# Optimization experiments

Hardware: AMD Instinct MI355X
Metric: run time of the kernel (lower is better)

Reference implementation:

```python
import jax, jax.numpy as jnp
import numpy as np

# Straight-through sign binarization (Binarize in BNN code mutates .data, so
# autograd sees identity -> custom_vjp with identity backward).
@jax.custom_vjp
def binarize(x):
    return jnp.sign(x)

def _bin_fwd(x):
    return jnp.sign(x), None

def _bin_bwd(_, g):
    return (g,)

binarize.defvjp(_bin_fwd, _bin_bwd)

EPS = 1e-5  # torch BatchNorm1d default eps

def batchnorm(x, g, b):
    # training-mode BN: batch statistics, biased variance
    if x.ndim == 3:  # (N, C, L): stats over N and L
        m = x.mean(axis=(0, 2), keepdims=True)
        v = x.var(axis=(0, 2), keepdims=True)
        return (x - m) / jnp.sqrt(v + EPS) * g[None, :, None] + b[None, :, None]
    m = x.mean(axis=0)
    v = x.var(axis=0)
    return (x - m) / jnp.sqrt(v + EPS) * g + b

def hardtanh(x):
    return jnp.clip(x, -1.0, 1.0)

def maxpool3(x):
    # MaxPool1d(kernel=3, stride=3): trim then reshape-max
    N, C, L = x.shape
    Lp = L // 3
    return x[:, :, :Lp * 3].reshape(N, C, Lp, 3).max(axis=-1)

def bconv(x, w, b, binarize_input=True):
    # BinarizeConv1d: kernel 41, dilation 2, VALID padding; weights sign-binarized,
    # inputs binarized except when in_channels == 3 (first layer rule in BNN code).
    xb = binarize(x) if binarize_input else x
    wb = binarize(w)
    y = jax.lax.conv_general_dilated(
        xb, wb, window_strides=(1,), padding='VALID',
        rhs_dilation=(2,), dimension_numbers=('NCH', 'OIH', 'NCH'))
    return y + b[None, :, None]

def blinear(x, w, b):
    # BinarizeLinear: in_features 832/1024 != 784 -> binarize input and weight
    return binarize(x) @ binarize(w).T + b

def _forward(x, bn0_g, bn0_b, conv1_w, conv1_b, bn1_g, bn1_b,
             conv2_w, conv2_b, bn2_g, bn2_b, conv3_w, conv3_b,
             bn3_g, bn3_b, conv4_w, conv4_b, bn4_g, bn4_b,
             conv5_w, conv5_b, fc1_w, fc1_b, bn5_g, bn5_b,
             fc2_w, fc2_b, bn6_g, bn6_b):
    h = hardtanh(batchnorm(x, bn0_g, bn0_b))
    h = maxpool3(bconv(h, conv1_w, conv1_b, binarize_input=False))  # (N,64,5306)
    h = hardtanh(batchnorm(h, bn1_g, bn1_b))
    h = maxpool3(bconv(h, conv2_w, conv2_b))  # (N,64,1742)
    h = hardtanh(batchnorm(h, bn2_g, bn2_b))
    h = maxpool3(bconv(h, conv3_w, conv3_b))  # (N,64,554)
    h = hardtanh(batchnorm(h, bn3_g, bn3_b))
    h = maxpool3(bconv(h, conv4_w, conv4_b))  # (N,64,158)
    h = hardtanh(batchnorm(h, bn4_g, bn4_b))
    h = maxpool3(bconv(h, conv5_w, conv5_b))  # (N,32,26)
    h = h.reshape(-1, 16 * 52)                # (N, 832)
    h = hardtanh(batchnorm(blinear(h, fc1_w, fc1_b), bn5_g, bn5_b))
    h = batchnorm(blinear(h, fc2_w, fc2_b), bn6_g, bn6_b)
    return jax.nn.log_softmax(h, axis=1)

def setup_inputs() -> dict:
    key = jax.random.key(0)
    ks = jax.random.split(key, 32)
    def rn(k, shape, s=0.1):
        return jax.random.normal(k, shape, dtype=jnp.float32) * s
    def bn_params(kg, kb, c):
        return 1.0 + rn(kg, (c,)), rn(kb, (c,))
    N, L, K = 64, 16000, 41
    d = {"x": jax.random.normal(ks[0], (N, 3, L), dtype=jnp.float32)}
    d["bn0_g"], d["bn0_b"] = bn_params(ks[1], ks[2], 3)
    d["conv1_w"], d["conv1_b"] = rn(ks[3], (64, 3, K)), rn(ks[4], (64,), 0.01)
    d["bn1_g"], d["bn1_b"] = bn_params(ks[5], ks[6], 64)
    d["conv2_w"], d["conv2_b"] = rn(ks[7], (64, 64, K)), rn(ks[8], (64,), 0.01)
    d["bn2_g"], d["bn2_b"] = bn_params(ks[9], ks[10], 64)
    d["conv3_w"], d["conv3_b"] = rn(ks[11], (64, 64, K)), rn(ks[12], (64,), 0.01)
    d["bn3_g"], d["bn3_b"] = bn_params(ks[13], ks[14], 64)
    d["conv4_w"], d["conv4_b"] = rn(ks[15], (64, 64, K)), rn(ks[16], (64,), 0.01)
    d["bn4_g"], d["bn4_b"] = bn_params(ks[17], ks[18], 64)
    d["conv5_w"], d["conv5_b"] = rn(ks[19], (32, 64, K)), rn(ks[20], (32,), 0.01)
    d["fc1_w"], d["fc1_b"] = rn(ks[21], (1024, 832)), rn(ks[22], (1024,), 0.01)
    d["bn5_g"], d["bn5_b"] = bn_params(ks[23], ks[24], 1024)
    d["fc2_w"], d["fc2_b"] = rn(ks[25], (1000, 1024)), rn(ks[26], (1000,), 0.01)
    d["bn6_g"], d["bn6_b"] = bn_params(ks[27], ks[28], 1000)
    return d

def reference(x, bn0_g, bn0_b, conv1_w, conv1_b, bn1_g, bn1_b,
              conv2_w, conv2_b, bn2_g, bn2_b, conv3_w, conv3_b,
              bn3_g, bn3_b, conv4_w, conv4_b, bn4_g, bn4_b,
              conv5_w, conv5_b, fc1_w, fc1_b, bn5_g, bn5_b,
              fc2_w, fc2_b, bn6_g, bn6_b):
    return _forward(x, bn0_g, bn0_b, conv1_w, conv1_b, bn1_g, bn1_b,
                    conv2_w, conv2_b, bn2_g, bn2_b, conv3_w, conv3_b,
                    bn3_g, bn3_b, conv4_w, conv4_b, bn4_g, bn4_b,
                    conv5_w, conv5_b, fc1_w, fc1_b, bn5_g, bn5_b,
                    fc2_w, fc2_b, bn6_g, bn6_b)
```

## Files before the change

### kernel.cpp

```cpp
#include <hip/hip_runtime.h>
#include <hip/hip_bf16.h>
#include <stdint.h>

typedef __hip_bfloat16 bf16;
typedef unsigned long long u64;
typedef unsigned short u16;

typedef __attribute__((ext_vector_type(8))) short bf16x8;
typedef __attribute__((ext_vector_type(4))) float f32x4;
typedef __attribute__((ext_vector_type(4))) int i32x4;

#define FIXCAP (1u << 20)
#define YQS 5312

static __device__ __forceinline__ float ldin(const void* p, long i, int f32) {
    return f32 ? ((const float*)p)[i] : __bfloat162float(((const bf16*)p)[i]);
}

static __device__ __forceinline__ i32x4 expand16_01(unsigned m) {
    union { int4 s; i32x4 v; } u;
    u.s.x = (int)((((m         & 0xFu) * 0x00204081u) & 0x01010101u));
    u.s.y = (int)((((m >> 4)  & 0xFu) * 0x00204081u) & 0x01010101u);
    u.s.z = (int)((((m >> 8)  & 0xFu) * 0x00204081u) & 0x01010101u);
    u.s.w = (int)((((m >> 12) & 0xFu) * 0x00204081u) & 0x01010101u);
    return u.v;
}

__global__ void k_probe(const void* x, unsigned* ctl) {
    int tid = threadIdx.x;
    int good = 0;
    for (int i = tid; i < 1024; i += 256) {
        float v = __bfloat162float(((const bf16*)x)[2 * i]);
        float a = fabsf(v);
        if (v == 0.0f || (isfinite(v) && a >= 1e-4f && a <= 100.0f)) good++;
    }
    __shared__ int s[256];
    s[tid] = good; __syncthreads();
    for (int st = 128; st > 0; st >>= 1) {
        if (tid < st) s[tid] += s[tid + st];
        __syncthreads();
    }
    if (tid == 0) { ctl[0] = 0u; ctl[1] = (s[0] >= 700) ? 0u : 1u; }
}

__global__ void k_sentinel(void* outv, const unsigned* ctl, float val) {
    int i = blockIdx.x * 256 + threadIdx.x;
    if (i >= 64000) return;
    if (ctl[1]) ((float*)outv)[i] = val;
    else ((bf16*)outv)[i] = __float2bfloat16(val);
}

__device__ __forceinline__ void pack_convw_task(const void* w, uint2* wp, int Co, int f32,
                                                int bx, int tid) {
    int t = bx * 256 + tid;
    if (t >= Co * 41) return;
    int co = t / 41, k = t % 41;
    unsigned w0 = 0, w1 = 0;
    for (int c = 0; c < 32; c++)
        if (ldin(w, (co * 64 + c) * 41 + k, f32) > 0.f) w0 |= (1u << c);
    for (int c = 0; c < 32; c++)
        if (ldin(w, (co * 64 + 32 + c) * 41 + k, f32) > 0.f) w1 |= (1u << c);
    wp[t] = make_uint2(w0, w1);
}
__device__ __forceinline__ void pack_rows_task(const void* w, unsigned* wp, int rows, int F,
                                               int f32, int bx, int tid) {
    int Fw = F >> 5;
    int t = bx * 256 + tid;
    if (t >= rows * Fw) return;
    int r = t / Fw, wi = t % Fw;
    unsigned m = 0;
    for (int j = 0; j < 32; j++)
        if (ldin(w, (long)r * F + wi * 32 + j, f32) > 0.f) m |= (1u << j);
    wp[t] = m;
}

__global__ void k_prep(const void* x, const void* c1w, const void* c2w, const void* c3w,
                       const void* c4w, const void* c5w, const void* f1w, const void* f2w,
                       u16* afrag, unsigned* wb, uint2* w3p, uint2* w4p, uint2* w5p,
                       unsigned* fc1wp, unsigned* fc2wp, u64* stats, double* part0,
                       const unsigned* ctl) {
    int f32 = ctl[1];
    int task = blockIdx.y, bx = blockIdx.x, tid = threadIdx.x;
    switch (task) {
        case 0: {
            int t = bx * 256 + tid;
            if (t < 2304) {
                int m = t / 576, rem = t - m * 576;
                int ks = rem / 64, lane = rem - ks * 64;
                int li = lane & 15, hq = lane >> 4;
                int row = 16 * m + li;
                int g = 4 * ks + hq;
                int c = g / 11, t0 = 4 * (g - 11 * c);
                u16* outp = afrag + (size_t)t * 8;
                for (int i2 = 0; i2 < 4; i2++) {
                    int tt = t0 + i2;
                    u16 sv = 0;
                    if (g < 33 && tt <= 40) {
                        float wv = ldin(c1w, (row * 3 + c) * 41 + tt, f32);
                        sv = (wv > 0.f) ? (u16)0x3F80 : ((wv < 0.f) ? (u16)0xBF80 : (u16)0);
                    }
                    outp[2 * i2] = sv;
                    outp[2 * i2 + 1] = sv;
                }
            }
        } break;
        case 1: {
            int t = bx * 256 + tid;
            if (t < 5248) {
                int lane = t & 63, g = t >> 6;
                int p = g & 1, tt = g >> 1;
                int li = lane & 15, hq = lane >> 4;
                unsigned d = 0;
#pragma unroll
                for (int mh = 0; mh < 2; mh++) {
                    int co = 16 * (2 * p + mh) + li;
                    unsigned msk = 0;
#pragma unroll
                    for (int j = 0; j < 16; j++) {
                        int c = 16 * hq + j;
                        if (ldin(c2w, (co * 64 + c) * 41 + tt, f32) > 0.f) msk |= 1u << j;
                    }
                    d |= msk << (16 * mh);
                }
                wb[t] = d;
            }
        } break;
        case 2: pack_convw_task(c3w, w3p, 64, f32, bx, tid); break;
        case 3: pack_convw_task(c4w, w4p, 64, f32, bx, tid); break;
        case 4: pack_convw_task(c5w, w5p, 32, f32, bx, tid); break;
        case 5: pack_rows_task(f1w, fc1wp, 1024, 832, f32, bx, tid); break;
        case 6: pack_rows_task(f2w, fc2wp, 1000, 1024, f32, bx, tid); break;
        case 7: {
            int i = bx * 256 + tid;
            if (i < 14400) stats[i] = 0ull;
        } break;
        case 8: {
            if (bx >= 96) return;
            int c = bx >> 5, s = bx & 31;
            double s1 = 0, s2 = 0;
            for (int n = 0; n < 64; n++) {
                long base = (long)(n * 3 + c) * 16000;
                for (int l = s * 256 + tid; l < 16000; l += 32 * 256) {
                    double v = (double)ldin(x, base + l, f32);
                    s1 += v; s2 += v * v;
                }
            }
            __shared__ double a1[256], a2[256];
            a1[tid] = s1; a2[tid] = s2;
            __syncthreads();
            for (int st = 128; st > 0; st >>= 1) {
                if (tid < st) { a1[tid] += a1[tid + st]; a2[tid] += a2[tid + st]; }
                __syncthreads();
            }
            if (tid == 0) { part0[(c * 32 + s) * 2] = a1[0]; part0[(c * 32 + s) * 2 + 1] = a2[0]; }
        } break;
    }
}

__global__ __launch_bounds__(256, 3) void k_conv1(const void* __restrict__ x,
                                                  const double* __restrict__ part0,
                                                  const void* __restrict__ g0,
                                                  const void* __restrict__ b0,
                                                  const u16* __restrict__ afrag,
                                                  float* __restrict__ yq,
                                                  double* __restrict__ yb,
                                                  const unsigned* __restrict__ ctl) {
    __shared__ unsigned xs[8][140];
    __shared__ float pool[4][48][20];
    __shared__ double sbuf[4][64][2];
    __shared__ float yst[16][68];
    __shared__ float2 b0f[3];
    int f32 = ctl[1];
    int n = blockIdx.y, bx = blockIdx.x, tid = threadIdx.x;
    if (tid < 3) {
        int c = tid;
        double s1 = 0, s2 = 0;
        for (int s = 0; s < 32; s++) { s1 += part0[(c * 32 + s) * 2]; s2 += part0[(c * 32 + s) * 2 + 1]; }
        double M = 64.0 * 16000.0;
        double mu = s1 / M, var = s2 / M - mu * mu;
        double A = (double)ldin(g0, c, f32) / sqrt(var + 1e-5);
        b0f[c] = make_float2((float)A, (float)((double)ldin(b0, c, f32) - mu * A));
    }
    __syncthreads();

    unsigned* xsf = &xs[0][0];
    for (int f = tid; f < 1120; f += 256) {
        int rc = f / 140, qi = f - rc * 140;
        int r = rc >> 2, c = rc & 3;
        unsigned dw = 0u;
        if (c < 3) {
            int xpos = 192 * bx + 2 * qi + r;
            if (xpos < 16000) {
                float2 pb = b0f[c];
                float v = fmaf(ldin(x, (long)(n * 3 + c) * 16000 + xpos, f32), pb.x, pb.y);
                v = fminf(fmaxf(v, -1.f), 1.f);
                bf16 h = __float2bfloat16(v);
                float hf = __bfloat162float(h);
                bf16 lo = __float2bfloat16(v - hf);
                dw = (unsigned)__bfloat16_as_ushort(h) | ((unsigned)__bfloat16_as_ushort(lo) << 16);
            }
        }
        xsf[f] = dw;
    }
    __syncthreads();

    int lane = tid & 63;
    int li = lane & 15, hq = lane >> 4;
    int w = __builtin_amdgcn_readfirstlane(tid >> 6);

    f32x4 zz = {0.f, 0.f, 0.f, 0.f};
    f32x4 acc[4][3];
#pragma unroll
    for (int m = 0; m < 4; m++)
#pragma unroll
        for (int nf = 0; nf < 3; nf++) acc[m][nf] = zz;

    int boff[3];
#pragma unroll
    for (int nf = 0; nf < 3; nf++) {
        int pl = 48 * w + 16 * nf + li;
        boff[nf] = (pl & 1) * 560 + (pl >> 1);
    }

    const bf16x8* ag = (const bf16x8*)afrag;
#pragma unroll 1
    for (int ks = 0; ks < 9; ks++) {
        int g = 4 * ks + hq;
        int c = g / 11;
        int kb = c * 140 + 4 * (g - 11 * c);
        bf16x8 a0 = ag[(0 * 9 + ks) * 64 + lane];
        bf16x8 a1 = ag[(1 * 9 + ks) * 64 + lane];
        bf16x8 a2 = ag[(2 * 9 + ks) * 64 + lane];
        bf16x8 a3 = ag[(3 * 9 + ks) * 64 + lane];
#pragma unroll
        for (int nf = 0; nf < 3; nf++) {
            const unsigned* bp = xsf + boff[nf] + kb;
            union { int4 i4; bf16x8 v; } u;
            u.i4 = make_int4(bp[0], bp[1], bp[2], bp[3]);
            acc[0][nf] = __builtin_amdgcn_mfma_f32_16x16x32_bf16(a0, u.v, acc[0][nf], 0, 0, 0);
            acc[1][nf] = __builtin_amdgcn_mfma_f32_16x16x32_bf16(a1, u.v, acc[1][nf], 0, 0, 0);
            acc[2][nf] = __builtin_amdgcn_mfma_f32_16x16x32_bf16(a2, u.v, acc[2][nf], 0, 0, 0);
            acc[3][nf] = __builtin_amdgcn_mfma_f32_16x16x32_bf16(a3, u.v, acc[3][nf], 0, 0, 0);
        }
    }

    int lp0 = 64 * bx + 16 * w;
#pragma unroll
    for (int m = 0; m < 4; m++) {
#pragma unroll
        for (int nf = 0; nf < 3; nf++)
            *(f32x4*)&pool[w][16 * nf + li][4 * hq] = acc[m][nf];
        double s = 0.0, q = 0.0;
        float mqv[4];
#pragma unroll
        for (int i = 0; i < 4; i++) {
            int pc = hq + 4 * i;
            float mq = fmaxf(fmaxf(pool[w][3 * pc][li], pool[w][3 * pc + 1][li]),
                             pool[w][3 * pc + 2][li]);
            mqv[i] = mq;
            if (lp0 + pc < 5306) {
                double d = (double)mq;
                s += d; q += d * d;
            }
        }
        s += __shfl_down(s, 32, 64); s += __shfl_down(s, 16, 64);
        q += __shfl_down(q, 32, 64); q += __shfl_down(q, 16, 64);
        if (lane < 16) { sbuf[w][16 * m + lane][0] = s; sbuf[w][16 * m + lane][1] = q; }
#pragma unroll
        for (int i = 0; i < 4; i++)
            yst[li][16 * w + hq + 4 * i] = mqv[i];
        __syncthreads();
        {
            int r = tid >> 4, c4 = (tid & 15) * 4;
            float4 v = *(const float4*)&yst[r][c4];
            *(float4*)&yq[((size_t)n * 64 + 16 * m + r) * YQS + 64 * bx + c4] = v;
        }
        __syncthreads();
    }
    if (tid < 64) {
        double s = sbuf[0][tid][0] + sbuf[1][tid][0] + sbuf[2][tid][0] + sbuf[3][tid][0];
        double q = sbuf[0][tid][1] + sbuf[1][tid][1] + sbuf[2][tid][1] + sbuf[3][tid][1];
        int sbk = bx & 15;
        atomicAdd(&yb[(tid * 16 + sbk) * 2], s);
        atomicAdd(&yb[(tid * 16 + sbk) * 2 + 1], q);
    }
}

__global__ void k_pack_y(const float* __restrict__ yq, const double* __restrict__ yb,
                         const void* g1, const void* b1,
                         uint2* __restrict__ xp,
                         unsigned* __restrict__ fixcnt, unsigned* __restrict__ fixlist,
                         const unsigned* __restrict__ ctl) {
    __shared__ double2 pqs[64];
    int f32 = ctl[1];
    int tid = threadIdx.x;
    if (tid < 64) {
        int c = tid;
        double s1 = 0, s2 = 0;
        for (int s = 0; s < 16; s++) { s1 += yb[(c * 16 + s) * 2]; s2 += yb[(c * 16 + s) * 2 + 1]; }
        double M = 64.0 * 5306.0;
        double mu = s1 / M;
        double var = s2 / M - mu * mu;
        double A = (double)ldin(g1, c, f32) / sqrt(var + 1e-5);
        pqs[c] = make_double2(A, (double)ldin(b1, c, f32) - mu * A);
    }
    __syncthreads();
    int n = blockIdx.y;
    int l = blockIdx.x * 256 + tid;
    if (l >= 5306) return;
    unsigned w0 = 0, w1 = 0;
    for (int c = 0; c < 64; c++) {
        double2 p = pqs[c];
        double v = (double)yq[((size_t)n * 64 + c) * YQS + l] * p.x + p.y;
        if (fabs(v) < 2e-3 * fabs(p.x)) {
            unsigned idx = atomicAdd(fixcnt, 1u);
            if (idx < FIXCAP) fixlist[idx] = ((unsigned)n << 19) | ((unsigned)c << 13) | (unsigned)l;
        }
        if (v > 0.0) { if (c < 32) w0 |= 1u << c; else w1 |= 1u << (c - 32); }
    }
    xp[(size_t)n * 5306 + l] = make_uint2(w0, w1);
}

__global__ void k_fix(const unsigned* __restrict__ fixcnt, const unsigned* __restrict__ fixlist,
                      const double* __restrict__ yb, const void* g1, const void* b1,
                      const void* __restrict__ x, const void* __restrict__ c1w,
                      const double* __restrict__ part0, const void* g0, const void* b0,
                      unsigned* __restrict__ x2p, const unsigned* __restrict__ ctl) {
    int f32 = ctl[1];
    unsigned cnt = min(*fixcnt, FIXCAP);
    for (unsigned t = blockIdx.x * 256 + threadIdx.x; t < cnt; t += gridDim.x * 256) {
        unsigned e = fixlist[t];
        int n = e >> 19, c = (e >> 13) & 63, l = e & 8191;
        double s1 = 0, s2 = 0;
        for (int s = 0; s < 16; s++) { s1 += yb[(c * 16 + s) * 2]; s2 += yb[(c * 16 + s) * 2 + 1]; }
        double M = 64.0 * 5306.0;
        double mu = s1 / M, var = s2 / M - mu * mu;
        double A = (double)ldin(g1, c, f32) / sqrt(var + 1e-5);
        double B = (double)ldin(b1, c, f32) - mu * A;
        double best = -1e300;
        for (int r = 0; r < 3; r++) {
            int pp = 3 * l + r;
            double acc = 0.0;
            for (int cc = 0; cc < 3; cc++) {
                double p1 = 0, p2 = 0;
                for (int s = 0; s < 32; s++) { p1 += part0[(cc * 32 + s) * 2]; p2 += part0[(cc * 32 + s) * 2 + 1]; }
                double M0 = 64.0 * 16000.0;
                double mu0 = p1 / M0, var0 = p2 / M0 - mu0 * mu0;
                double A0 = (double)ldin(g0, cc, f32) / sqrt(var0 + 1e-5);
                double B0 = (double)ldin(b0, cc, f32) - mu0 * A0;
                for (int k = 0; k < 41; k++) {
                    float wf = ldin(c1w, (c * 3 + cc) * 41 + k, f32);
                    double sgn = (wf > 0.f) ? 1.0 : ((wf < 0.f) ? -1.0 : 0.0);
                    double xv = (double)ldin(x, (long)(n * 3 + cc) * 16000 + pp + 2 * k, f32);
                    xv = fmin(fmax(xv * A0 + B0, -1.0), 1.0);
                    acc = fma(sgn, xv, acc);
                }
            }
            best = fmax(best, acc);
        }
        double v = best * A + B;
        unsigned* word = &x2p[((size_t)n * 5306 + l) * 2 + (c >> 5)];
        unsigned bit = 1u << (c & 31);
        if (v > 0.0) atomicOr(word, bit);
        else atomicAnd(word, ~bit);
    }
}

__global__ __launch_bounds__(256, 3) void k_conv_i8(const uint2* __restrict__ xp,
                                                    const unsigned* __restrict__ wb,
                                                    u16* __restrict__ mout,
                                                    u64* __restrict__ stat, int nbase) {
    __shared__ __align__(16) char arena[44608];
    unsigned* xsd = (unsigned*)arena;
    unsigned* wlds = (unsigned*)(arena + 21760);
    int* Tarr = (int*)(arena + 42752);
    int* csA  = (int*)(arena + 43520);
    int n = nbase + blockIdx.y, bx = blockIdx.x, tid = threadIdx.x;
    int base = 192 * bx;

    for (int i = tid; i < 5248; i += 256) wlds[i] = wb[i];

    for (int e = tid; e < 272; e += 256) {
        int pos = base + e;
        int r = e & 1, qi = e >> 1;
        unsigned* dst = xsd + (r * 136 + qi) * 20;
        unsigned d[16];
        int cs = 0;
        if (pos < 5306) {
            uint2 mk = xp[(size_t)n * 5306 + pos];
            cs = 2 * (__popc(mk.x) + __popc(mk.y)) - 64;
#pragma unroll
            for (int dw = 0; dw < 8; dw++) {
                unsigned nib = (mk.x >> (4 * dw)) & 0xFu;
                unsigned sp = (nib * 0x00204081u) & 0x01010101u;
                d[dw] = ~(sp * 0xFEu);
            }
#pragma unroll
            for (int dw = 0; dw < 8; dw++) {
                unsigned nib = (mk.y >> (4 * dw)) & 0xFu;
                unsigned sp = (nib * 0x00204081u) & 0x01010101u;
                d[8 + dw] = ~(sp * 0xFEu);
            }
        } else {
#pragma unroll
            for (int dw = 0; dw < 16; dw++) d[dw] = 0u;
        }
#pragma unroll
        for (int v4 = 0; v4 < 4; v4++)
            *(uint4*)(dst + 4 * v4) = make_uint4(d[4 * v4], d[4 * v4 + 1],
                                                 d[4 * v4 + 2], d[4 * v4 + 3]);
        csA[r * 136 + qi] = cs;
    }
    __syncthreads();

    if (tid < 192) {
        int r = tid & 1, q = tid >> 1;
        int s = 0;
        for (int k = 0; k < 41; k++) s += csA[r * 136 + q + k];
        Tarr[tid] = s;
    }

    int lane = tid & 63;
    int li = lane & 15, hq = lane >> 4;
    int w = __builtin_amdgcn_readfirstlane(tid >> 6);

    i32x4 zz = {0, 0, 0, 0};
    i32x4 acc[4][3];
#pragma unroll
    for (int m = 0; m < 4; m++)
#pragma unroll
        for (int nf = 0; nf < 3; nf++) acc[m][nf] = zz;

    int boff[3];
#pragma unroll
    for (int nf = 0; nf < 3; nf++) {
        int pl = 48 * w + 16 * nf + li;
        boff[nf] = ((pl & 1) * 136 + (pl >> 1)) * 80 + 16 * hq;
    }

    const char* xsb = (const char*)xsd;
    const unsigned* wl = wlds + lane;

#pragma unroll 1
    for (int t = 0; t < 41; t++) {
        unsigned w01 = wl[(t * 2 + 0) * 64];
        unsigned w23 = wl[(t * 2 + 1) * 64];
        i32x4 a0 = expand16_01(w01 & 0xFFFFu);
        i32x4 a1 = expand16_01(w01 >> 16);
        i32x4 a2 = expand16_01(w23 & 0xFFFFu);
        i32x4 a3 = expand16_01(w23 >> 16);
#pragma unroll
        for (int nf = 0; nf < 3; nf++) {
            i32x4 b = *(const i32x4*)(xsb + boff[nf] + t * 80);
            acc[0][nf] = __builtin_amdgcn_mfma_i32_16x16x64_i8(a0, b, acc[0][nf], 0, 0, 0);
            acc[1][nf] = __builtin_amdgcn_mfma_i32_16x16x64_i8(a1, b, acc[1][nf], 0, 0, 0);
            acc[2][nf] = __builtin_amdgcn_mfma_i32_16x16x64_i8(a2, b, acc[2][nf], 0, 0, 0);
            acc[3][nf] = __builtin_amdgcn_mfma_i32_16x16x64_i8(a3, b, acc[3][nf], 0, 0, 0);
        }
    }

    __syncthreads();
    int (*pooli)[48][20] = (int (*)[48][20])arena;
    u16 (*mt)[72] = (u16 (*)[72])(arena + 15360);
    int sbk = bx & 15;
#pragma unroll
    for (int m = 0; m < 4; m++) {
#pragma unroll
        for (int nf = 0; nf < 3; nf++)
            *(i32x4*)&pooli[w][16 * nf + li][4 * hq] = acc[m][nf];
        int c = 16 * m + li;
        unsigned s = 0, q = 0;
#pragma unroll
        for (int i = 0; i < 4; i++) {
            int pc = hq + 4 * i;
            int d0 = 2 * pooli[w][3 * pc][li]     - Tarr[48 * w + 3 * pc];
            int d1 = 2 * pooli[w][3 * pc + 1][li] - Tarr[48 * w + 3 * pc + 1];
            int d2 = 2 * pooli[w][3 * pc + 2][li] - Tarr[48 * w + 3 * pc + 2];
            int d = max(max(d0, d1), d2);
            int mv = (2624 - d) >> 1;
            mt[c][16 * w + pc] = (u16)mv;
            int lp = 64 * bx + 16 * w + pc;
            if (lp < 1742) {
                s += (unsigned)mv;
                q += (unsigned)(mv * mv);
            }
        }
        s += __shfl_down(s, 32, 64); s += __shfl_down(s, 16, 64);
        q += __shfl_down(q, 32, 64); q += __shfl_down(q, 16, 64);
        if (lane < 16) {
            atomicAdd(&stat[((16 * m + lane) * 16 + sbk) * 2], (u64)s);
            atomicAdd(&stat[((16 * m + lane) * 16 + sbk) * 2 + 1], (u64)q);
        }
    }
    __syncthreads();
    {
        int c = tid >> 2, seg = tid & 3;
        int lp0 = 64 * bx + seg * 16;
        size_t rowb = ((size_t)n * 64 + c) * 1742;
        const u16* mp = &mt[c][seg * 16];
        if (lp0 + 15 < 1742) {
            unsigned* op = (unsigned*)(mout + rowb + lp0);
#pragma unroll
            for (int j = 0; j < 8; j++)
                op[j] = (unsigned)mp[2 * j] | ((unsigned)mp[2 * j + 1] << 16);
        } else {
            for (int j = 0; j < 16; j++) {
                int lp = lp0 + j;
                if (lp < 1742) mout[rowb + lp] = mp[j];
            }
        }
    }
}

__global__ __launch_bounds__(256) void k_conv_binm(const u16* __restrict__ min_,
                                                   const u64* __restrict__ statIn,
                                                   const void* g, const void* b, double M,
                                                   const uint2* __restrict__ wp,
                                                   u16* __restrict__ mout,
                                                   u64* __restrict__ statOut,
                                                   int Lp, int Lin, int Co,
                                                   const unsigned* __restrict__ ctl) {
    __shared__ double2 pqs[64];
    __shared__ uint2 xt[272];
    int f32 = ctl[1];
    int n = blockIdx.y, tid = threadIdx.x;
    if (tid < 64) {
        int c = tid;
        u64 s1 = 0, s2 = 0;
        for (int s = 0; s < 16; s++) { s1 += statIn[(c * 16 + s) * 2]; s2 += statIn[(c * 16 + s) * 2 + 1]; }
        double mu = (double)s1 / M;
        double varm = (double)s2 / M - mu * mu;
        double A = (double)ldin(g, c, f32) / sqrt(4.0 * varm + 1e-5);
        pqs[c] = make_double2(-2.0 * A, 2.0 * A * mu + (double)ldin(b, c, f32));
    }
    __syncthreads();
    int base = blockIdx.x * 192;
    for (int i = tid; i < 272; i += 256) {
        int pos = base + i;
        unsigned w0 = 0, w1 = 0;
        if (pos < Lin) {
            const u16* mp = min_ + (size_t)n * 64 * Lin + pos;
#pragma unroll 4
            for (int c = 0; c < 32; c++) {
                double2 p = pqs[c];
                if ((double)mp[(size_t)c * Lin] * p.x + p.y > 0.0) w0 |= 1u << c;
            }
#pragma unroll 4
            for (int c = 0; c < 32; c++) {
                double2 p = pqs[c + 32];
                if ((double)mp[(size_t)(c + 32) * Lin] * p.x + p.y > 0.0) w1 |= 1u << c;
            }
        }
        xt[i] = make_uint2(w0, w1);
    }
    __syncthreads();

    int lane = tid & 63;
    int wave = __builtin_amdgcn_readfirstlane(tid >> 6);
    int co0 = blockIdx.z * 32 + wave * 8;
    int lp = blockIdx.x * 64 + lane;

    int acc[8][3] = {};
    uint2 xa = xt[3 * lane];
    for (int k = 0; k < 41; k++) {
        uint2 xb = xt[3 * lane + 2 * k + 1];
        uint2 xc = xt[3 * lane + 2 * k + 2];
#pragma unroll
        for (int j = 0; j < 8; j++) {
            uint2 w = wp[(co0 + j) * 41 + k];
            acc[j][0] += __popc(w.x ^ xa.x) + __popc(w.y ^ xa.y);
            acc[j][1] += __popc(w.x ^ xb.x) + __popc(w.y ^ xb.y);
            acc[j][2] += __popc(w.x ^ xc.x) + __popc(w.y ^ xc.y);
        }
        xa = xc;
    }
    bool ok = lp < Lp;
    int sb = blockIdx.x & 15;
#pragma unroll
    for (int j = 0; j < 8; j++) {
        int m = min(min(acc[j][0], acc[j][1]), acc[j][2]);
        if (ok) mout[((size_t)n * 64 + co0 + j) * Lp + lp] = (u16)m;
        if (statOut) {
            unsigned s = ok ? (unsigned)m : 0u;
            unsigned q = ok ? (unsigned)(m * m) : 0u;
            for (int off = 32; off > 0; off >>= 1) {
                s += __shfl_down(s, off, 64);
                q += __shfl_down(q, off, 64);
            }
            if (lane == 0) {
                atomicAdd(&statOut[((co0 + j) * 16 + sb) * 2], (u64)s);
                atomicAdd(&statOut[((co0 + j) * 16 + sb) * 2 + 1], (u64)q);
            }
        }
    }
}

__global__ void k_c5fc1(const u16* __restrict__ m4, const u64* __restrict__ s4,
                        const void* g4, const void* b4,
                        const uint2* __restrict__ w5p, const void* __restrict__ b5,
                        const unsigned* __restrict__ fc1wp, u16* __restrict__ acc1,
                        u64* __restrict__ s5, const unsigned* __restrict__ ctl) {
    __shared__ double2 pqs[64];
    __shared__ uint2 xt[280];
    __shared__ int m5s[32][26];
    __shared__ unsigned xw[26];
    int f32 = ctl[1];
    int n = blockIdx.x, tid = threadIdx.x;
    const int Lin = 158;
    if (tid < 64) {
        int c = tid;
        u64 s1 = 0, s2 = 0;
        for (int s = 0; s < 16; s++) { s1 += s4[(c * 16 + s) * 2]; s2 += s4[(c * 16 + s) * 2 + 1]; }
        double M = 64.0 * 158.0;
        double mu = (double)s1 / M;
        double varm = (double)s2 / M - mu * mu;
        double A = (double)ldin(g4, c, f32) / sqrt(4.0 * varm + 1e-5);
        pqs[c] = make_double2(-2.0 * A, 2.0 * A * mu + (double)ldin(b4, c, f32));
    }
    __syncthreads();
    for (int i = tid; i < 280; i += 256) {
        unsigned w0 = 0, w1 = 0;
        if (i < Lin) {
            const u16* mp = m4 + (size_t)n * 64 * Lin + i;
#pragma unroll 4
            for (int c = 0; c < 32; c++) {
                double2 p = pqs[c];
                if ((double)mp[(size_t)c * Lin] * p.x + p.y > 0.0) w0 |= 1u << c;
            }
#pragma unroll 4
            for (int c = 0; c < 32; c++) {
                double2 p = pqs[c + 32];
                if ((double)mp[(size_t)(c + 32) * Lin] * p.x + p.y > 0.0) w1 |= 1u << c;
            }
        }
        xt[i] = make_uint2(w0, w1);
    }
    __syncthreads();

    int lane = tid & 63;
    int wave = __builtin_amdgcn_readfirstlane(tid >> 6);
    int co0 = wave * 8;
    int acc[8][3] = {};
    uint2 xa = xt[3 * lane];
    for (int k = 0; k < 41; k++) {
        uint2 xb = xt[3 * lane + 2 * k + 1];
        uint2 xc = xt[3 * lane + 2 * k + 2];
#pragma unroll
        for (int j = 0; j < 8; j++) {
            uint2 w = w5p[(co0 + j) * 41 + k];
            acc[j][0] += __popc(w.x ^ xa.x) + __popc(w.y ^ xa.y);
            acc[j][1] += __popc(w.x ^ xb.x) + __popc(w.y ^ xb.y);
            acc[j][2] += __popc(w.x ^ xc.x) + __popc(w.y ^ xc.y);
        }
        xa = xc;
    }
    if (lane < 26) {
#pragma unroll
        for (int j = 0; j < 8; j++)
            m5s[co0 + j][lane] = min(min(acc[j][0], acc[j][1]), acc[j][2]);
    }
    __syncthreads();
    if (tid < 26) {
        unsigned mask = 0;
        for (int j = 0; j < 32; j++) {
            int f = tid * 32 + j, c = f / 26, l = f % 26;
            double yv = 2624.0 - 2.0 * (double)m5s[c][l] + (double)ldin(b5, c, f32);
            if (yv > 0.0) mask |= 1u << j;
        }
        xw[tid] = mask;
    }
    __syncthreads();
#pragma unroll
    for (int i = 0; i < 4; i++) {
        int j = tid + i * 256;
        unsigned a = 0;
        for (int w = 0; w < 26; w++) a += __popc(xw[w] ^ fc1wp[j * 26 + w]);
        acc1[n * 1024 + j] = (u16)a;
        atomicAdd(&s5[j * 2], (u64)a);
        atomicAdd(&s5[j * 2 + 1], (u64)(a * a));
    }
}

__global__ void k_fc2(const u16* __restrict__ acc1, const u64* __restrict__ s5,
                      const void* g5, const void* b5, const unsigned* __restrict__ fc2wp,
                      u16* __restrict__ acc2, u64* __restrict__ s6, const unsigned* ctl) {
    __shared__ double2 pq5s[1024];
    __shared__ unsigned xw[32];
    int f32 = ctl[1];
    int n = blockIdx.y, tid = threadIdx.x;
    for (int f = tid; f < 1024; f += 256) {
        u64 a1 = s5[f * 2], a2 = s5[f * 2 + 1];
        double mu = (double)a1 / 64.0;
        double varm = (double)a2 / 64.0 - mu * mu;
        double A = (double)ldin(g5, f, f32) / sqrt(4.0 * varm + 1e-5);
        pq5s[f] = make_double2(-2.0 * A, 2.0 * A * mu + (double)ldin(b5, f, f32));
    }
    __syncthreads();
    if (tid < 32) {
        unsigned mask = 0;
        for (int j = 0; j < 32; j++) {
            int f = tid * 32 + j;
            double2 p = pq5s[f];
            if ((double)acc1[n * 1024 + f] * p.x + p.y > 0.0) mask |= 1u << j;
        }
        xw[tid] = mask;
    }
    __syncthreads();
    int j = blockIdx.x * 256 + tid;
    if (j >= 1000) return;
    unsigned a = 0;
    for (int w = 0; w < 32; w++) a += __popc(xw[w] ^ fc2wp[j * 32 + w]);
    acc2[n * 1000 + j] = (u16)a;
    atomicAdd(&s6[j * 2], (u64)a);
    atomicAdd(&s6[j * 2 + 1], (u64)(a * a));
}

__global__ void k_lsm(const u16* __restrict__ acc2, const u64* __restrict__ s6,
                      const void* g6, const void* b6, const unsigned* ctl, void* outv) {
    int n = blockIdx.x, tid = threadIdx.x;
    int f32 = ctl[1];
    __shared__ double red[256];
    double v[4];
    double mx = -1e300;
#pragma unroll
    for (int i = 0; i < 4; i++) {
        int j = tid + i * 256;
        if (j < 1000) {
            u64 a1 = s6[j * 2], a2 = s6[j * 2 + 1];
            double mu = (double)a1 / 64.0;
            double varm = (double)a2 / 64.0 - mu * mu;
            double A = (double)ldin(g6, j, f32) / sqrt(4.0 * varm + 1e-5);
            v[i] = (double)acc2[n * 1000 + j] * (-2.0 * A) + (2.0 * A * mu + (double)ldin(b6, j, f32));
            mx = fmax(mx, v[i]);
        } else v[i] = -1e300;
    }
    red[tid] = mx; __syncthreads();
    for (int s = 128; s > 0; s >>= 1) {
        if (tid < s) red[tid] = fmax(red[tid], red[tid + s]);
        __syncthreads();
    }
    mx = red[0]; __syncthreads();
    double sum = 0.0;
#pragma unroll
    for (int i = 0; i < 4; i++) {
        int j = tid + i * 256;
        if (j < 1000) sum += exp(v[i] - mx);
    }
    red[tid] = sum; __syncthreads();
    for (int s = 128; s > 0; s >>= 1) {
        if (tid < s) red[tid] += red[tid + s];
        __syncthreads();
    }
    double ls = log(red[0]);
#pragma unroll
    for (int i = 0; i < 4; i++) {
        int j = tid + i * 256;
        if (j < 1000) {
            float r = (float)(v[i] - mx - ls);
            if (!isfinite(r)) r = -700.0f;
            if (f32) ((float*)outv)[n * 1000 + j] = r;
            else ((bf16*)outv)[n * 1000 + j] = __float2bfloat16(r);
        }
    }
}

extern "C" void kernel_launch(void* const* d_in, const int* in_sizes, int n_in,
                              void* d_out, int out_size, void* d_ws, size_t ws_size,
                              hipStream_t stream) {
    const void* x       = d_in[0];
    const void* bn0_g   = d_in[1];
    const void* bn0_b   = d_in[2];
    const void* conv1_w = d_in[3];
    const void* bn1_g   = d_in[5];
    const void* bn1_b   = d_in[6];
    const void* conv2_w = d_in[7];
    const void* bn2_g   = d_in[9];
    const void* bn2_b   = d_in[10];
    const void* conv3_w = d_in[11];
    const void* bn3_g   = d_in[13];
    const void* bn3_b   = d_in[14];
    const void* conv4_w = d_in[15];
    const void* bn4_g   = d_in[17];
    const void* bn4_b   = d_in[18];
    const void* conv5_w = d_in[19];
    const void* conv5_b = d_in[20];
    const void* fc1_w   = d_in[21];
    const void* bn5_g   = d_in[23];
    const void* bn5_b   = d_in[24];
    const void* fc2_w   = d_in[25];
    const void* bn6_g   = d_in[27];
    const void* bn6_b   = d_in[28];

    char* wsb = (char*)d_ws;
    size_t off = 0;
    auto alloc = [&](size_t bytes) -> void* {
        off = (off + 255) & ~(size_t)255;
        void* p = wsb + off;
        off += bytes;
        return p;
    };

    unsigned* ctl   = (unsigned*)alloc(256);
    unsigned* x2p   = (unsigned*)alloc(2716672);
    float*    yq    = (float*)alloc((size_t)64 * 64 * YQS * 4);
    u16*      m2    = (u16*)alloc(14270464);
    u16*      m3    = (u16*)alloc(4538368);
    u16*      m4    = (u16*)alloc(1294336);
    u16*      acc1  = (u16*)alloc(131072);
    u16*      acc2  = (u16*)alloc(128000);
    u16*      afrag = (u16*)alloc(36864);
    unsigned* wb    = (unsigned*)alloc(20992);
    uint2*    w3p   = (uint2*)alloc(20992);
    uint2*    w4p   = (uint2*)alloc(20992);
    uint2*    w5p   = (uint2*)alloc(10496);
    unsigned* fc1wp = (unsigned*)alloc(106496);
    unsigned* fc2wp = (unsigned*)alloc(128000);
    u64*      stats = (u64*)alloc(14400 * 8);
    double*   part0 = (double*)alloc(2048);
    unsigned* fixlist = (unsigned*)alloc(FIXCAP * 4);
    size_t need = (off + 255) & ~(size_t)255;

    u64* s2 = stats;
    u64* s3 = stats + 2048;
    u64* s4 = stats + 4096;
    u64* s5 = stats + 6144;
    u64* s6 = stats + 8192;
    double* yb = (double*)(stats + 12288);
    unsigned* fixcnt = (unsigned*)(stats + 14340);

    k_probe<<<1, 256, 0, stream>>>(x, ctl);

    if (n_in != 29) {
        k_sentinel<<<250, 256, 0, stream>>>(d_out, ctl, -(3000.0f + (float)n_in));
        return;
    }
    if (ws_size < need) {
        k_sentinel<<<250, 256, 0, stream>>>(d_out, ctl, -1500.0f);
        return;
    }

    k_prep<<<dim3(125, 9), 256, 0, stream>>>(x, conv1_w, conv2_w, conv3_w, conv4_w, conv5_w,
                                             fc1_w, fc2_w, afrag, wb, w3p, w4p, w5p,
                                             fc1wp, fc2wp, stats, part0, ctl);

    k_conv1<<<dim3(83, 64), 256, 0, stream>>>(x, part0, bn0_g, bn0_b, afrag, yq, yb, ctl);
    k_pack_y<<<dim3(21, 64), 256, 0, stream>>>(yq, yb, bn1_g, bn1_b, (uint2*)x2p,
                                               fixcnt, fixlist, ctl);
    k_fix<<<64, 256, 0, stream>>>(fixcnt, fixlist, yb, bn1_g, bn1_b, x, conv1_w,
                                  part0, bn0_g, bn0_b, x2p, ctl);

    k_conv_i8<<<dim3(28, 32), 256, 0, stream>>>((const uint2*)x2p, wb, m2, s2, 0);
    k_conv_i8<<<dim3(28, 32), 256, 0, stream>>>((const uint2*)x2p, wb, m2, s2, 32);
    k_conv_binm<<<dim3(9, 64, 2), 256, 0, stream>>>(m2, s2, bn2_g, bn2_b, 64.0 * 1742.0,
                                                    w3p, m3, s3, 554, 1742, 64, ctl);
    k_conv_binm<<<dim3(3, 64, 2), 256, 0, stream>>>(m3, s3, bn3_g, bn3_b, 64.0 * 554.0,
                                                    w4p, m4, s4, 158, 554, 64, ctl);

    k_c5fc1<<<64, 256, 0, stream>>>(m4, s4, bn4_g, bn4_b, w5p, conv5_b, fc1wp, acc1, s5, ctl);
    k_fc2<<<dim3(4, 64), 256, 0, stream>>>(acc1, s5, bn5_g, bn5_b, fc2wp, acc2, s6, ctl);
    k_lsm<<<64, 256, 0, stream>>>(acc2, s6, bn6_g, bn6_b, ctl, d_out);
}
```

Before: 750.0 us.

## Parallelize fixup per wavefront with precomputed BN params; merge conv_i8 launches

The fixup kernel now computes BN1 and BN0 scale/shift once per block into shared memory instead of recomputing them per entry, and assigns one 64-lane wavefront per fix entry, splitting the 123 taps across lanes and reducing with shuffles. The grid is doubled to 128 blocks. The two half-batch conv_i8 launches are merged into one 64-row launch to cut launch overhead and fill the GPU. The cost is shuffle reductions and idle lanes when the fix list is short.

```diff
diff --git a/kernel.cpp b/kernel.cpp
--- a/kernel.cpp
+++ b/kernel.cpp
@@ -321,48 +321,70 @@
     xp[(size_t)n * 5306 + l] = make_uint2(w0, w1);
 }
 
-__global__ void k_fix(const unsigned* __restrict__ fixcnt, const unsigned* __restrict__ fixlist,
-                      const double* __restrict__ yb, const void* g1, const void* b1,
-                      const void* __restrict__ x, const void* __restrict__ c1w,
-                      const double* __restrict__ part0, const void* g0, const void* b0,
-                      unsigned* __restrict__ x2p, const unsigned* __restrict__ ctl) {
+__global__ __launch_bounds__(256) void k_fix(const unsigned* __restrict__ fixcnt,
+                                             const unsigned* __restrict__ fixlist,
+                                             const double* __restrict__ yb,
+                                             const void* g1, const void* b1,
+                                             const void* __restrict__ x,
+                                             const void* __restrict__ c1w,
+                                             const double* __restrict__ part0,
+                                             const void* g0, const void* b0,
+                                             unsigned* __restrict__ x2p,
+                                             const unsigned* __restrict__ ctl) {
+    __shared__ double2 pqs[64];
+    __shared__ double2 p0s[3];
     int f32 = ctl[1];
+    int tid = threadIdx.x;
+    if (tid < 64) {
+        double s1 = 0, s2 = 0;
+        for (int s = 0; s < 16; s++) { s1 += yb[(tid * 16 + s) * 2]; s2 += yb[(tid * 16 + s) * 2 + 1]; }
+        double M = 64.0 * 5306.0;
+        double mu = s1 / M, var = s2 / M - mu * mu;
+        double A = (double)ldin(g1, tid, f32) / sqrt(var + 1e-5);
+        pqs[tid] = make_double2(A, (double)ldin(b1, tid, f32) - mu * A);
+    } else if (tid < 67) {
+        int cc = tid - 64;
+        double p1 = 0, p2 = 0;
+        for (int s = 0; s < 32; s++) { p1 += part0[(cc * 32 + s) * 2]; p2 += part0[(cc * 32 + s) * 2 + 1]; }
+        double M0 = 64.0 * 16000.0;
+        double mu0 = p1 / M0, var0 = p2 / M0 - mu0 * mu0;
+        double A0 = (double)ldin(g0, cc, f32) / sqrt(var0 + 1e-5);
+        p0s[cc] = make_double2(A0, (double)ldin(b0, cc, f32) - mu0 * A0);
+    }
+    __syncthreads();
     unsigned cnt = min(*fixcnt, FIXCAP);
-    for (unsigned t = blockIdx.x * 256 + threadIdx.x; t < cnt; t += gridDim.x * 256) {
+    int lane = tid & 63;
+    int wid = blockIdx.x * 4 + (tid >> 6);
+    int nw = gridDim.x * 4;
+    for (unsigned t = wid; t < cnt; t += nw) {
         unsigned e = fixlist[t];
         int n = e >> 19, c = (e >> 13) & 63, l = e & 8191;
-        double s1 = 0, s2 = 0;
-        for (int s = 0; s < 16; s++) { s1 += yb[(c * 16 + s) * 2]; s2 += yb[(c * 16 + s) * 2 + 1]; }
-        double M = 64.0 * 5306.0;
-        double mu = s1 / M, var = s2 / M - mu * mu;
-        double A = (double)ldin(g1, c, f32) / sqrt(var + 1e-5);
-        double B = (double)ldin(b1, c, f32) - mu * A;
         double best = -1e300;
+#pragma unroll 1
         for (int r = 0; r < 3; r++) {
             int pp = 3 * l + r;
             double acc = 0.0;
-            for (int cc = 0; cc < 3; cc++) {
-                double p1 = 0, p2 = 0;
-                for (int s = 0; s < 32; s++) { p1 += part0[(cc * 32 + s) * 2]; p2 += part0[(cc * 32 + s) * 2 + 1]; }
-                double M0 = 64.0 * 16000.0;
-                double mu0 = p1 / M0, var0 = p2 / M0 - mu0 * mu0;
-                double A0 = (double)ldin(g0, cc, f32) / sqrt(var0 + 1e-5);
-                double B0 = (double)ldin(b0, cc, f32) - mu0 * A0;
-                for (int k = 0; k < 41; k++) {
-                    float wf = ldin(c1w, (c * 3 + cc) * 41 + k, f32);
-                    double sgn = (wf > 0.f) ? 1.0 : ((wf < 0.f) ? -1.0 : 0.0);
-                    double xv = (double)ldin(x, (long)(n * 3 + cc) * 16000 + pp + 2 * k, f32);
-                    xv = fmin(fmax(xv * A0 + B0, -1.0), 1.0);
-                    acc = fma(sgn, xv, acc);
-                }
-            }
+            for (int i = lane; i < 123; i += 64) {
+                int cc = i / 41, k = i - cc * 41;
+                float wf = ldin(c1w, (c * 3 + cc) * 41 + k, f32);
+                double sgn = (wf > 0.f) ? 1.0 : ((wf < 0.f) ? -1.0 : 0.0);
+                double2 P0 = p0s[cc];
+                double xv = (double)ldin(x, (long)(n * 3 + cc) * 16000 + pp + 2 * k, f32);
+                xv = fmin(fmax(xv * P0.x + P0.y, -1.0), 1.0);
+                acc = fma(sgn, xv, acc);
+            }
+            for (int off = 32; off > 0; off >>= 1) acc += __shfl_down(acc, off, 64);
+            acc = __shfl(acc, 0, 64);
             best = fmax(best, acc);
         }
-        double v = best * A + B;
-        unsigned* word = &x2p[((size_t)n * 5306 + l) * 2 + (c >> 5)];
-        unsigned bit = 1u << (c & 31);
-        if (v > 0.0) atomicOr(word, bit);
-        else atomicAnd(word, ~bit);
+        if (lane == 0) {
+            double2 P = pqs[c];
+            double v = best * P.x + P.y;
+            unsigned* word = &x2p[((size_t)n * 5306 + l) * 2 + (c >> 5)];
+            unsigned bit = 1u << (c & 31);
+            if (v > 0.0) atomicOr(word, bit);
+            else atomicAnd(word, ~bit);
+        }
     }
 }
 
@@ -846,11 +868,10 @@
     k_conv1<<<dim3(83, 64), 256, 0, stream>>>(x, part0, bn0_g, bn0_b, afrag, yq, yb, ctl);
     k_pack_y<<<dim3(21, 64), 256, 0, stream>>>(yq, yb, bn1_g, bn1_b, (uint2*)x2p,
                                                fixcnt, fixlist, ctl);
-    k_fix<<<64, 256, 0, stream>>>(fixcnt, fixlist, yb, bn1_g, bn1_b, x, conv1_w,
-                                  part0, bn0_g, bn0_b, x2p, ctl);
-
-    k_conv_i8<<<dim3(28, 32), 256, 0, stream>>>((const uint2*)x2p, wb, m2, s2, 0);
-    k_conv_i8<<<dim3(28, 32), 256, 0, stream>>>((const uint2*)x2p, wb, m2, s2, 32);
+    k_fix<<<128, 256, 0, stream>>>(fixcnt, fixlist, yb, bn1_g, bn1_b, x, conv1_w,
+                                   part0, bn0_g, bn0_b, x2p, ctl);
+
+    k_conv_i8<<<dim3(28, 64), 256, 0, stream>>>((const uint2*)x2p, wb, m2, s2, 0);
     k_conv_binm<<<dim3(9, 64, 2), 256, 0, stream>>>(m2, s2, bn2_g, bn2_b, 64.0 * 1742.0,
                                                     w3p, m3, s3, 554, 1742, 64, ctl);
     k_conv_binm<<<dim3(3, 64, 2), 256, 0, stream>>>(m3, s3, bn3_g, bn3_b, 64.0 * 554.0,
```

New measurement: 652.0 us. 13.1% less time.
